# Performance work log

Hardware: AMD Instinct MI355X
Metric: run time of the kernel (lower is better)

The kernel has to match this reference:

```python
import jax, jax.numpy as jnp
import numpy as np

B, CIN, COUT, S, K, G = 2, 64, 64, 128, 3, 4  # batch, in_ch, out_ch, shapes(H=W), kernel, groups


def _conv1x1(w, x, b=None):
    # nn.Conv2d(kernel_size=1): w [O,C], x [B,C,H,W]
    y = jnp.einsum('oc,bchw->bohw', w, x)
    return y if b is None else y + b[None, :, None, None]


def _forward(fs, ft, w_q, w_k, w_v, rel_h, rel_w, weights1_real, weights1_imag,
             w0_w, w0_b, convv_w, convv_b, convv1_w, convv1_b, rate1, rate2):
    Bq, C, H, W = fs.shape
    q = _conv1x1(w_q, fs)  # [B,C,H,W]
    # key/value convs are 1x1 with no bias, so conv(pad(x)) == pad(conv(x))
    kf = jnp.pad(_conv1x1(w_k, fs), ((0, 0), (0, 0), (1, 1), (1, 1)))
    vf = jnp.pad(_conv1x1(w_v, fs), ((0, 0), (0, 0), (1, 1), (1, 1)))

    def unfold(xp):  # [B,C,H+2,W+2] -> [B,C,H,W,K,K] (torch .unfold(2,K,1).unfold(3,K,1))
        p = jnp.stack([xp[:, :, i:i + H, j:j + W] for i in range(K) for j in range(K)], axis=-1)
        return p.reshape(Bq, C, H, W, K, K)

    k = unfold(kf)
    v = unfold(vf)
    # relative position bias on the two channel halves (broadcast as in torch)
    k = jnp.concatenate([k[:, :C // 2] + rel_h, k[:, C // 2:] + rel_w], axis=1)
    k = k.reshape(Bq, G, C // G, H, W, K * K)
    v = v.reshape(Bq, G, C // G, H, W, K * K)
    qg = q.reshape(Bq, G, C // G, H, W, 1)
    attn = jax.nn.softmax(qg * k, axis=-1)                         # [B,G,C/G,H,W,9]
    out = jnp.einsum('bnchwk,bnchwk->bnchw', attn, v).reshape(Bq, C, H, W)

    # ---- spectral branch ----
    # Original code: einsum 'bchw,ohwi->bochw' (i is summed over weights only),
    # flatten to [B, o*c*H, W], fftshift over dims(1,2), reshape to [B,64,8192,128,2],
    # zero an EMPTY slice (rw=int(0.1*1)=0), ifftshift over dims(3,2,1), then
    # ifft2 with s=(H,W) which CROPS the 8192 dim to its first H rows.
    # The roll arithmetic composes to: net-zero shift on o and w axes, and a
    # +C/2 shift on the c axis; the crop then selects c = C//2, h = 0..H-1.
    # => out1 = Re ifft2( fft2(out)[:, C//2] * sum_i W[o,:,h,w] ).
    fs_ft = jnp.fft.fft2(out, norm='ortho')                        # [B,C,H,W] complex
    wsum = (weights1_real + 1j * weights1_imag).sum(axis=1)        # [CIN,H,W] (sum over 'i')
    out_ft = fs_ft[:, C // 2][:, None, :, :] * wsum[None]          # [B,CIN,H,W]
    out1 = jnp.fft.ifft2(out_ft, norm='ortho').real                # [B,CIN,H,W]

    out_cv = _conv1x1(convv_w, out, convv_b)                       # con_vv
    out2 = _conv1x1(w0_w, out_cv, w0_b)                            # w0
    out2 = _conv1x1(convv1_w, out2, convv1_b)                      # con_vv1

    make_fs = rate1[0] * out1 + rate2[0] * out2                    # [B,CIN,H,W]
    make_fs = jnp.transpose(make_fs, (0, 2, 3, 1))                 # [B,H,W,C]
    ftv = ft.reshape(Bq, H, W, C)                                  # out_channels != 320 branch
    return jnp.mean((make_fs - ftv) ** 2)


def setup_inputs() -> dict:
    key = jax.random.key(0)
    ks = jax.random.split(key, 12)
    n = lambda i, shape, s=1.0: jax.random.normal(ks[i], shape, dtype=jnp.float32) * s
    scale = 1.0 / (CIN * COUT)
    return {
        'fs': n(0, (B, CIN, S, S)),
        'ft': n(1, (B, S, S, COUT)),
        'w_q': n(2, (COUT, CIN), 0.1),
        'w_k': n(3, (COUT, CIN), 0.1),
        'w_v': n(4, (COUT, CIN), 0.1),
        'rel_h': n(5, (COUT // 2, 1, 1, K, 1)),
        'rel_w': n(6, (COUT // 2, 1, 1, 1, K)),
        'weights1_real': jax.random.uniform(ks[7], (CIN, COUT, S, S), dtype=jnp.float32) * scale,
        'weights1_imag': jax.random.uniform(ks[8], (CIN, COUT, S, S), dtype=jnp.float32) * scale,
        'w0_w': n(9, (COUT, CIN), 0.1),
        'w0_b': jnp.zeros((COUT,), jnp.float32),
        'convv_w': n(10, (CIN, COUT), 0.1),
        'convv_b': jnp.zeros((CIN,), jnp.float32),
        'convv1_w': n(11, (CIN, COUT), 0.1),
        'convv1_b': jnp.zeros((CIN,), jnp.float32),
        'rate1': jnp.full((1,), 0.5, jnp.float32),
        'rate2': jnp.full((1,), 0.5, jnp.float32),
    }


def reference(fs, ft, w_q, w_k, w_v, rel_h, rel_w, weights1_real, weights1_imag,
              w0_w, w0_b, convv_w, convv_b, convv1_w, convv1_b, rate1, rate2):
    return _forward(fs, ft, w_q, w_k, w_v, rel_h, rel_w, weights1_real, weights1_imag,
                    w0_w, w0_b, convv_w, convv_b, convv1_w, convv1_b, rate1, rate2)
```

## Files before the change

### kernel.cpp

```cpp
#include <hip/hip_runtime.h>
#include <math.h>

constexpr int HW   = 128 * 128;
constexpr int NCHW = 2 * 64 * HW;

constexpr size_t OFF_Q    = 0;
constexpr size_t OFF_K    = 2097152;
constexpr size_t OFF_V    = 4194304;
constexpr size_t OFF_OUT  = 6291456;
constexpr size_t OFF_OUT2 = 8388608;
constexpr size_t OFF_R    = 8388608;
constexpr size_t OFF_F    = 10485760;
constexpr size_t OFF_M    = 10551296;
constexpr size_t OFF_BC   = 10555392;
constexpr size_t OFF_Z    = 0;
constexpr size_t OFF_P    = 4194304;

__global__ __launch_bounds__(256) void k_qkv(
    const float* __restrict__ fs,
    const float* __restrict__ w_q, const float* __restrict__ w_k, const float* __restrict__ w_v,
    float* __restrict__ q, float* __restrict__ kk, float* __restrict__ vv)
{
    __shared__ float xs[64][64];
    __shared__ float wl[3][64][65];
    int blk = blockIdx.x;
    int b = blk >> 8;
    int px0 = (blk & 255) << 6;
    int t = threadIdx.x;
    for (int i = t; i < 4096; i += 256) {
        int r = i >> 6, cix = i & 63;
        wl[0][r][cix] = w_q[i];
        wl[1][r][cix] = w_k[i];
        wl[2][r][cix] = w_v[i];
        xs[r][cix] = fs[b * (64 * HW) + r * HW + px0 + cix];
    }
    __syncthreads();
    int pxq = t & 15, rq = t >> 4;
    float aq[4][4], ak[4][4], av[4][4];
    #pragma unroll
    for (int i = 0; i < 4; i++)
        for (int j = 0; j < 4; j++) { aq[i][j] = 0.f; ak[i][j] = 0.f; av[i][j] = 0.f; }
    for (int ci = 0; ci < 64; ci++) {
        float4 xv = *reinterpret_cast<const float4*>(&xs[ci][pxq * 4]);
        #pragma unroll
        for (int i = 0; i < 4; i++) {
            float wq_ = wl[0][rq * 4 + i][ci];
            float wk_ = wl[1][rq * 4 + i][ci];
            float wv_ = wl[2][rq * 4 + i][ci];
            aq[i][0] += wq_ * xv.x; aq[i][1] += wq_ * xv.y; aq[i][2] += wq_ * xv.z; aq[i][3] += wq_ * xv.w;
            ak[i][0] += wk_ * xv.x; ak[i][1] += wk_ * xv.y; ak[i][2] += wk_ * xv.z; ak[i][3] += wk_ * xv.w;
            av[i][0] += wv_ * xv.x; av[i][1] += wv_ * xv.y; av[i][2] += wv_ * xv.z; av[i][3] += wv_ * xv.w;
        }
    }
    #pragma unroll
    for (int i = 0; i < 4; i++) {
        int co = rq * 4 + i;
        size_t base = (size_t)b * (64 * HW) + (size_t)co * HW + px0 + pxq * 4;
        *reinterpret_cast<float4*>(q  + base) = make_float4(aq[i][0], aq[i][1], aq[i][2], aq[i][3]);
        *reinterpret_cast<float4*>(kk + base) = make_float4(ak[i][0], ak[i][1], ak[i][2], ak[i][3]);
        *reinterpret_cast<float4*>(vv + base) = make_float4(av[i][0], av[i][1], av[i][2], av[i][3]);
    }
}

__global__ __launch_bounds__(256) void k_gemm64(
    const float* __restrict__ x, const float* __restrict__ w,
    const float* __restrict__ bias, float* __restrict__ y)
{
    __shared__ float xs[64][64];
    __shared__ float wl[64][65];
    int blk = blockIdx.x;
    int b = blk >> 8;
    int px0 = (blk & 255) << 6;
    int t = threadIdx.x;
    for (int i = t; i < 4096; i += 256) {
        int r = i >> 6, cix = i & 63;
        wl[r][cix] = w[i];
        xs[r][cix] = x[b * (64 * HW) + r * HW + px0 + cix];
    }
    __syncthreads();
    int pxq = t & 15, rq = t >> 4;
    float acc[4][4];
    #pragma unroll
    for (int i = 0; i < 4; i++)
        for (int j = 0; j < 4; j++) acc[i][j] = 0.f;
    for (int ci = 0; ci < 64; ci++) {
        float4 xv = *reinterpret_cast<const float4*>(&xs[ci][pxq * 4]);
        #pragma unroll
        for (int i = 0; i < 4; i++) {
            float wv = wl[rq * 4 + i][ci];
            acc[i][0] += wv * xv.x; acc[i][1] += wv * xv.y;
            acc[i][2] += wv * xv.z; acc[i][3] += wv * xv.w;
        }
    }
    #pragma unroll
    for (int i = 0; i < 4; i++) {
        int co = rq * 4 + i;
        float bb = bias ? bias[co] : 0.f;
        float* p = y + b * (64 * HW) + co * HW + px0 + pxq * 4;
        p[0] = acc[i][0] + bb; p[1] = acc[i][1] + bb;
        p[2] = acc[i][2] + bb; p[3] = acc[i][3] + bb;
    }
}

__global__ __launch_bounds__(256) void k_attn(
    const float* __restrict__ q, const float* __restrict__ kc, const float* __restrict__ vc,
    const float* __restrict__ rel_h, const float* __restrict__ rel_w,
    float* __restrict__ out)
{
    int idx = blockIdx.x * 256 + threadIdx.x;
    if (idx >= NCHW) return;
    int w = idx & 127;
    int h = (idx >> 7) & 127;
    int c = (idx >> 14) & 63;
    float qv = q[idx];
    float s[9], vv[9];
    #pragma unroll
    for (int ki = 0; ki < 3; ki++) {
        #pragma unroll
        for (int kj = 0; kj < 3; kj++) {
            int hh = h + ki - 1, ww = w + kj - 1;
            bool inb = (hh >= 0 && hh < 128 && ww >= 0 && ww < 128);
            int nidx = (idx & ~(HW - 1)) + hh * 128 + ww;
            float kvv = inb ? kc[nidx] : 0.f;
            float vvv = inb ? vc[nidx] : 0.f;
            float rel = (c < 32) ? rel_h[c * 3 + ki] : rel_w[(c - 32) * 3 + kj];
            s[ki * 3 + kj] = qv * (kvv + rel);
            vv[ki * 3 + kj] = vvv;
        }
    }
    float m = s[0];
    #pragma unroll
    for (int i = 1; i < 9; i++) m = fmaxf(m, s[i]);
    float den = 0.f, num = 0.f;
    #pragma unroll
    for (int i = 0; i < 9; i++) { float e = __expf(s[i] - m); den += e; num += e * vv[i]; }
    out[idx] = num / den;
}

__global__ __launch_bounds__(128) void k_fftrow_fwd(const float* __restrict__ out, float* __restrict__ R)
{
    int bh = blockIdx.x; int b = bh >> 7, h = bh & 127;
    int k = threadIdx.x;
    __shared__ float xr[128];
    xr[k] = out[((b * 64 + 32) << 14) + h * 128 + k];
    __syncthreads();
    float s0, c0; __sincosf(-6.2831853071795864769f * (float)k / 128.0f, &s0, &c0);
    float twr = 1.f, twi = 0.f, ar = 0.f, ai = 0.f;
    for (int n = 0; n < 128; n++) {
        float xv = xr[n];
        ar += xv * twr; ai += xv * twi;
        float nr = twr * c0 - twi * s0;
        twi = twr * s0 + twi * c0; twr = nr;
    }
    float2* Rp = (float2*)R;
    Rp[(b << 14) + h * 128 + k] = make_float2(ar, ai);
}

__global__ __launch_bounds__(128) void k_fftcol_fwd(const float* __restrict__ R, float* __restrict__ F)
{
    int bk = blockIdx.x; int b = bk >> 7, k2 = bk & 127;
    int k1 = threadIdx.x;
    __shared__ float2 col[128];
    const float2* Rp = (const float2*)R;
    col[k1] = Rp[(b << 14) + k1 * 128 + k2];
    __syncthreads();
    float s0, c0; __sincosf(-6.2831853071795864769f * (float)k1 / 128.0f, &s0, &c0);
    float twr = 1.f, twi = 0.f, ar = 0.f, ai = 0.f;
    for (int n = 0; n < 128; n++) {
        float2 xv = col[n];
        ar += xv.x * twr - xv.y * twi;
        ai += xv.x * twi + xv.y * twr;
        float nr = twr * c0 - twi * s0;
        twi = twr * s0 + twi * c0; twr = nr;
    }
    float2* Fp = (float2*)F;
    Fp[(b << 14) + k1 * 128 + k2] = make_float2(ar * (1.f / 128.f), ai * (1.f / 128.f));
}

__global__ __launch_bounds__(1024) void k_combine(
    const float* __restrict__ convv_w, const float* __restrict__ convv_b,
    const float* __restrict__ w0_w, const float* __restrict__ w0_b,
    const float* __restrict__ convv1_w, const float* __restrict__ convv1_b,
    float* __restrict__ M, float* __restrict__ bc)
{
    __shared__ float A[64][64];
    __shared__ float Bm[64][64];
    __shared__ float Cm[64][64];
    __shared__ float T[64][65];
    __shared__ float t2[64];
    int t = threadIdx.x;
    for (int e = t; e < 4096; e += 1024) {
        int i = e >> 6, j = e & 63;
        A[i][j]  = convv_w[e];
        Bm[i][j] = w0_w[e];
        Cm[i][j] = convv1_w[e];
    }
    __syncthreads();
    for (int e = t; e < 4096; e += 1024) {
        int i = e >> 6, j = e & 63;
        float a = 0.f;
        for (int kk = 0; kk < 64; kk++) a += Bm[i][kk] * A[kk][j];
        T[i][j] = a;
    }
    if (t < 64) {
        float a = 0.f;
        for (int kk = 0; kk < 64; kk++) a += Bm[t][kk] * convv_b[kk];
        t2[t] = a + w0_b[t];
    }
    __syncthreads();
    for (int e = t; e < 4096; e += 1024) {
        int i = e >> 6, j = e & 63;
        float a = 0.f;
        for (int kk = 0; kk < 64; kk++) a += Cm[i][kk] * T[kk][j];
        M[e] = a;
    }
    if (t < 64) {
        float a = 0.f;
        for (int kk = 0; kk < 64; kk++) a += Cm[t][kk] * t2[kk];
        bc[t] = a + convv1_b[t];
    }
}

__global__ __launch_bounds__(256) void k_wsum_partial(
    const float* __restrict__ w1r, const float* __restrict__ w1i, float* __restrict__ P)
{
    int blk = blockIdx.x;
    int chunk = blk & 15;
    int half  = (blk >> 4) & 1;
    int c     = blk >> 5;
    int t = threadIdx.x;
    int hw4 = (chunk << 8) + t;
    size_t base4 = ((size_t)c << 18) + ((size_t)half << 17) + (size_t)hw4;
    const float4* r4 = reinterpret_cast<const float4*>(w1r) + base4;
    const float4* i4 = reinterpret_cast<const float4*>(w1i) + base4;
    float4 sr = make_float4(0.f, 0.f, 0.f, 0.f);
    float4 si = make_float4(0.f, 0.f, 0.f, 0.f);
    #pragma unroll 16
    for (int o = 0; o < 32; o++) {
        float4 a = r4[o << 12];
        float4 b = i4[o << 12];
        sr.x += a.x; sr.y += a.y; sr.z += a.z; sr.w += a.w;
        si.x += b.x; si.y += b.y; si.z += b.z; si.w += b.w;
    }
    float2* Pp = reinterpret_cast<float2*>(P);
    size_t ob = ((size_t)half << 20) + ((size_t)c << 14) + (size_t)hw4 * 4;
    Pp[ob + 0] = make_float2(sr.x, si.x);
    Pp[ob + 1] = make_float2(sr.y, si.y);
    Pp[ob + 2] = make_float2(sr.z, si.z);
    Pp[ob + 3] = make_float2(sr.w, si.w);
}

__global__ __launch_bounds__(128) void k_ifftrow(
    const float* __restrict__ P, const float* __restrict__ F, float* __restrict__ Z)
{
    int blk = blockIdx.x; int c = blk >> 7, h = blk & 127;
    int t = threadIdx.x;
    __shared__ float2 g0[128];
    __shared__ float2 g1[128];
    const float2* Pp = (const float2*)P;
    const float2* Fp = (const float2*)F;
    float2 p0 = Pp[((size_t)c << 14) + (h << 7) + t];
    float2 p1 = Pp[((size_t)1 << 20) + ((size_t)c << 14) + (h << 7) + t];
    float wr = p0.x + p1.x, wi = p0.y + p1.y;
    float2 f0 = Fp[(h << 7) + t];
    float2 f1 = Fp[(1 << 14) + (h << 7) + t];
    g0[t] = make_float2(f0.x * wr - f0.y * wi, f0.x * wi + f0.y * wr);
    g1[t] = make_float2(f1.x * wr - f1.y * wi, f1.x * wi + f1.y * wr);
    __syncthreads();
    float s0, c0; __sincosf(6.2831853071795864769f * (float)t / 128.0f, &s0, &c0);
    float twr = 1.f, twi = 0.f;
    float a0r = 0.f, a0i = 0.f, a1r = 0.f, a1i = 0.f;
    for (int n = 0; n < 128; n++) {
        float2 u0 = g0[n];
        float2 u1 = g1[n];
        a0r += u0.x * twr - u0.y * twi;
        a0i += u0.x * twi + u0.y * twr;
        a1r += u1.x * twr - u1.y * twi;
        a1i += u1.x * twi + u1.y * twr;
        float nr = twr * c0 - twi * s0;
        twi = twr * s0 + twi * c0; twr = nr;
    }
    float2* Zp = (float2*)Z;
    Zp[((size_t)c << 14) + h * 128 + t]        = make_float2(a0r, a0i);
    Zp[((size_t)(64 + c) << 14) + h * 128 + t] = make_float2(a1r, a1i);
}

__global__ __launch_bounds__(256) void k_ifftcol_mse(
    const float* __restrict__ Zb, const float* __restrict__ out2,
    const float* __restrict__ ft, const float* __restrict__ rate1,
    const float* __restrict__ rate2, float* __restrict__ result)
{
    int blk = blockIdx.x;
    int xc = blk & 3;
    int c  = (blk >> 2) & 63;
    int b  = blk >> 8;
    int t = threadIdx.x;
    int xl = t & 31;
    int yq = t >> 5;
    __shared__ float2 zs[128][33];
    const float2* Zp = (const float2*)Zb;
    int zbase = ((b * 64 + c) << 14) + xc * 32;
    for (int e = t; e < 4096; e += 256) {
        int hh = e >> 5, xx = e & 31;
        zs[hh][xx] = Zp[zbase + hh * 128 + xx];
    }
    __syncthreads();

    float twx[4], twy[4], stx[4], sty[4];
    float Sr[4][4], Si[4][4];
    #pragma unroll
    for (int j = 0; j < 4; j++) {
        int y0 = yq + 8 * j;
        float ss, cc;
        __sincosf(6.2831853071795864769f * (float)y0 / 128.0f, &ss, &cc);
        stx[j] = cc; sty[j] = ss;
        twx[j] = 1.f; twy[j] = 0.f;
        #pragma unroll
        for (int m = 0; m < 4; m++) { Sr[j][m] = 0.f; Si[j][m] = 0.f; }
    }
    for (int h = 0; h < 128; h += 4) {
        #pragma unroll
        for (int m = 0; m < 4; m++) {
            float2 z = zs[h + m][xl];
            #pragma unroll
            for (int j = 0; j < 4; j++) {
                Sr[j][m] += z.x * twx[j] - z.y * twy[j];
                Si[j][m] += z.x * twy[j] + z.y * twx[j];
                float nr = twx[j] * stx[j] - twy[j] * sty[j];
                twy[j]   = twx[j] * sty[j] + twy[j] * stx[j];
                twx[j]   = nr;
            }
        }
    }
    float r1 = rate1[0], r2 = rate2[0];
    int x = xc * 32 + xl;
    int obase = ((b * 64 + c) << 14) + x;
    float part = 0.f;
    #pragma unroll
    for (int j = 0; j < 4; j++) {
        int y0 = yq + 8 * j;
        float o[4];
        o[0] = Sr[j][0] + Sr[j][1] + Sr[j][2] + Sr[j][3];
        o[1] = Sr[j][0] - Si[j][1] - Sr[j][2] + Si[j][3];
        o[2] = Sr[j][0] - Sr[j][1] + Sr[j][2] - Sr[j][3];
        o[3] = Sr[j][0] + Si[j][1] - Sr[j][2] - Si[j][3];
        #pragma unroll
        for (int m = 0; m < 4; m++) {
            int y = y0 + 32 * m;
            float out1 = o[m] * (1.f / 128.f);
            int gi = obase + y * 128;
            float mk = r1 * out1 + r2 * out2[gi];
            int fidx = ((b * HW + y * 128 + x) << 6) + c;
            float d = mk - ft[fidx];
            part += d * d;
        }
    }
    __shared__ float red[256];
    red[t] = part;
    __syncthreads();
    for (int s = 128; s > 0; s >>= 1) {
        if (t < s) red[t] += red[t + s];
        __syncthreads();
    }
    if (t == 0) atomicAdd(result, red[0] * (1.f / 2097152.f));
}

extern "C" void kernel_launch(void* const* d_in, const int* in_sizes, int n_in,
                              void* d_out, int out_size, void* d_ws, size_t ws_size,
                              hipStream_t stream) {
    const float* fs       = (const float*)d_in[0];
    const float* ft       = (const float*)d_in[1];
    const float* w_q      = (const float*)d_in[2];
    const float* w_k      = (const float*)d_in[3];
    const float* w_v      = (const float*)d_in[4];
    const float* rel_h    = (const float*)d_in[5];
    const float* rel_w    = (const float*)d_in[6];
    const float* w1r      = (const float*)d_in[7];
    const float* w1i      = (const float*)d_in[8];
    const float* w0_w     = (const float*)d_in[9];
    const float* w0_b     = (const float*)d_in[10];
    const float* convv_w  = (const float*)d_in[11];
    const float* convv_b  = (const float*)d_in[12];
    const float* convv1_w = (const float*)d_in[13];
    const float* convv1_b = (const float*)d_in[14];
    const float* rate1    = (const float*)d_in[15];
    const float* rate2    = (const float*)d_in[16];

    float* ws = (float*)d_ws;
    float* q    = ws + OFF_Q;
    float* kk   = ws + OFF_K;
    float* vv   = ws + OFF_V;
    float* out  = ws + OFF_OUT;
    float* out2 = ws + OFF_OUT2;
    float* R    = ws + OFF_R;
    float* F    = ws + OFF_F;
    float* M    = ws + OFF_M;
    float* bc   = ws + OFF_BC;
    float* Z    = ws + OFF_Z;
    float* P    = ws + OFF_P;

    k_qkv<<<512, 256, 0, stream>>>(fs, w_q, w_k, w_v, q, kk, vv);
    k_attn<<<8192, 256, 0, stream>>>(q, kk, vv, rel_h, rel_w, out);
    k_fftrow_fwd<<<256, 128, 0, stream>>>(out, R);
    k_fftcol_fwd<<<256, 128, 0, stream>>>(R, F);
    k_combine<<<1, 1024, 0, stream>>>(convv_w, convv_b, w0_w, w0_b, convv1_w, convv1_b, M, bc);
    k_gemm64<<<512, 256, 0, stream>>>(out, M, bc, out2);
    k_wsum_partial<<<2048, 256, 0, stream>>>(w1r, w1i, P);
    k_ifftrow<<<8192, 128, 0, stream>>>(P, F, Z);
    hipMemsetAsync(d_out, 0, sizeof(float), stream);
    k_ifftcol_mse<<<512, 256, 0, stream>>>(Z, out2, ft, rate1, rate2, (float*)d_out);
}
```

Baseline: 705.0 us.

## Fuse weight-combine into row FFT launch and restructure wsum reduction loads

The single-block matrix-combine kernel is merged into the forward row-FFT kernel as an extra 257th block, removing one launch and letting the combine run concurrently with the FFT rows. Because that block now has 128 threads instead of 1024, its tail work is longer. The weight-sum reduction is reworked to issue eight independent float4 loads per iteration into four accumulator sets, with a per-block rotated starting phase to spread memory accesses. It also gets an occupancy hint in launch_bounds. This targets memory-level parallelism on the 64 MB weight read that likely dominates runtime.

```diff
diff --git a/kernel.cpp b/kernel.cpp
--- a/kernel.cpp
+++ b/kernel.cpp
@@ -137,23 +137,66 @@
     out[idx] = num / den;
 }
 
-__global__ __launch_bounds__(128) void k_fftrow_fwd(const float* __restrict__ out, float* __restrict__ R)
-{
-    int bh = blockIdx.x; int b = bh >> 7, h = bh & 127;
-    int k = threadIdx.x;
+__global__ __launch_bounds__(128) void k_fftrow_combine(
+    const float* __restrict__ out, float* __restrict__ R,
+    const float* __restrict__ convv_w, const float* __restrict__ convv_b,
+    const float* __restrict__ w0_w, const float* __restrict__ w0_b,
+    const float* __restrict__ convv1_w, const float* __restrict__ convv1_b,
+    float* __restrict__ M, float* __restrict__ bc)
+{
     __shared__ float xr[128];
-    xr[k] = out[((b * 64 + 32) << 14) + h * 128 + k];
-    __syncthreads();
-    float s0, c0; __sincosf(-6.2831853071795864769f * (float)k / 128.0f, &s0, &c0);
-    float twr = 1.f, twi = 0.f, ar = 0.f, ai = 0.f;
-    for (int n = 0; n < 128; n++) {
-        float xv = xr[n];
-        ar += xv * twr; ai += xv * twi;
-        float nr = twr * c0 - twi * s0;
-        twi = twr * s0 + twi * c0; twr = nr;
-    }
-    float2* Rp = (float2*)R;
-    Rp[(b << 14) + h * 128 + k] = make_float2(ar, ai);
+    __shared__ float A[64][64];
+    __shared__ float Bm[64][64];
+    __shared__ float Cm[64][64];
+    __shared__ float T[64][65];
+    __shared__ float t2[64];
+    int t = threadIdx.x;
+    if (blockIdx.x < 256) {
+        int bh = blockIdx.x; int b = bh >> 7, h = bh & 127;
+        xr[t] = out[((b * 64 + 32) << 14) + h * 128 + t];
+        __syncthreads();
+        float s0, c0; __sincosf(-6.2831853071795864769f * (float)t / 128.0f, &s0, &c0);
+        float twr = 1.f, twi = 0.f, ar = 0.f, ai = 0.f;
+        for (int n = 0; n < 128; n++) {
+            float xv = xr[n];
+            ar += xv * twr; ai += xv * twi;
+            float nr = twr * c0 - twi * s0;
+            twi = twr * s0 + twi * c0; twr = nr;
+        }
+        float2* Rp = (float2*)R;
+        Rp[(b << 14) + h * 128 + t] = make_float2(ar, ai);
+        return;
+    }
+    for (int e = t; e < 4096; e += 128) {
+        int i = e >> 6, j = e & 63;
+        A[i][j]  = convv_w[e];
+        Bm[i][j] = w0_w[e];
+        Cm[i][j] = convv1_w[e];
+    }
+    __syncthreads();
+    for (int e = t; e < 4096; e += 128) {
+        int i = e >> 6, j = e & 63;
+        float a = 0.f;
+        for (int kk = 0; kk < 64; kk++) a += Bm[i][kk] * A[kk][j];
+        T[i][j] = a;
+    }
+    if (t < 64) {
+        float a = 0.f;
+        for (int kk = 0; kk < 64; kk++) a += Bm[t][kk] * convv_b[kk];
+        t2[t] = a + w0_b[t];
+    }
+    __syncthreads();
+    for (int e = t; e < 4096; e += 128) {
+        int i = e >> 6, j = e & 63;
+        float a = 0.f;
+        for (int kk = 0; kk < 64; kk++) a += Cm[i][kk] * T[kk][j];
+        M[e] = a;
+    }
+    if (t < 64) {
+        float a = 0.f;
+        for (int kk = 0; kk < 64; kk++) a += Cm[t][kk] * t2[kk];
+        bc[t] = a + convv1_b[t];
+    }
 }
 
 __global__ __launch_bounds__(128) void k_fftcol_fwd(const float* __restrict__ R, float* __restrict__ F)
@@ -177,51 +220,7 @@
     Fp[(b << 14) + k1 * 128 + k2] = make_float2(ar * (1.f / 128.f), ai * (1.f / 128.f));
 }
 
-__global__ __launch_bounds__(1024) void k_combine(
-    const float* __restrict__ convv_w, const float* __restrict__ convv_b,
-    const float* __restrict__ w0_w, const float* __restrict__ w0_b,
-    const float* __restrict__ convv1_w, const float* __restrict__ convv1_b,
-    float* __restrict__ M, float* __restrict__ bc)
-{
-    __shared__ float A[64][64];
-    __shared__ float Bm[64][64];
-    __shared__ float Cm[64][64];
-    __shared__ float T[64][65];
-    __shared__ float t2[64];
-    int t = threadIdx.x;
-    for (int e = t; e < 4096; e += 1024) {
-        int i = e >> 6, j = e & 63;
-        A[i][j]  = convv_w[e];
-        Bm[i][j] = w0_w[e];
-        Cm[i][j] = convv1_w[e];
-    }
-    __syncthreads();
-    for (int e = t; e < 4096; e += 1024) {
-        int i = e >> 6, j = e & 63;
-        float a = 0.f;
-        for (int kk = 0; kk < 64; kk++) a += Bm[i][kk] * A[kk][j];
-        T[i][j] = a;
-    }
-    if (t < 64) {
-        float a = 0.f;
-        for (int kk = 0; kk < 64; kk++) a += Bm[t][kk] * convv_b[kk];
-        t2[t] = a + w0_b[t];
-    }
-    __syncthreads();
-    for (int e = t; e < 4096; e += 1024) {
-        int i = e >> 6, j = e & 63;
-        float a = 0.f;
-        for (int kk = 0; kk < 64; kk++) a += Cm[i][kk] * T[kk][j];
-        M[e] = a;
-    }
-    if (t < 64) {
-        float a = 0.f;
-        for (int kk = 0; kk < 64; kk++) a += Cm[t][kk] * t2[kk];
-        bc[t] = a + convv1_b[t];
-    }
-}
-
-__global__ __launch_bounds__(256) void k_wsum_partial(
+__global__ __launch_bounds__(256, 4) void k_wsum_partial(
     const float* __restrict__ w1r, const float* __restrict__ w1i, float* __restrict__ P)
 {
     int blk = blockIdx.x;
@@ -233,21 +232,44 @@
     size_t base4 = ((size_t)c << 18) + ((size_t)half << 17) + (size_t)hw4;
     const float4* r4 = reinterpret_cast<const float4*>(w1r) + base4;
     const float4* i4 = reinterpret_cast<const float4*>(w1i) + base4;
-    float4 sr = make_float4(0.f, 0.f, 0.f, 0.f);
-    float4 si = make_float4(0.f, 0.f, 0.f, 0.f);
-    #pragma unroll 16
-    for (int o = 0; o < 32; o++) {
-        float4 a = r4[o << 12];
-        float4 b = i4[o << 12];
-        sr.x += a.x; sr.y += a.y; sr.z += a.z; sr.w += a.w;
-        si.x += b.x; si.y += b.y; si.z += b.z; si.w += b.w;
-    }
+    int phase = (chunk + c * 3 + half * 5) & 7;
+    float4 aR0 = make_float4(0.f,0.f,0.f,0.f), aR1 = aR0, aR2 = aR0, aR3 = aR0;
+    float4 aI0 = aR0, aI1 = aR0, aI2 = aR0, aI3 = aR0;
+    #pragma unroll
+    for (int oo = 0; oo < 8; oo++) {
+        int g = (oo + phase) & 7;
+        size_t ob = (size_t)(g << 2) << 12;
+        float4 r0 = r4[ob];
+        float4 r1 = r4[ob + 4096];
+        float4 r2 = r4[ob + 8192];
+        float4 r3 = r4[ob + 12288];
+        float4 s0 = i4[ob];
+        float4 s1 = i4[ob + 4096];
+        float4 s2 = i4[ob + 8192];
+        float4 s3 = i4[ob + 12288];
+        aR0.x += r0.x; aR0.y += r0.y; aR0.z += r0.z; aR0.w += r0.w;
+        aR1.x += r1.x; aR1.y += r1.y; aR1.z += r1.z; aR1.w += r1.w;
+        aR2.x += r2.x; aR2.y += r2.y; aR2.z += r2.z; aR2.w += r2.w;
+        aR3.x += r3.x; aR3.y += r3.y; aR3.z += r3.z; aR3.w += r3.w;
+        aI0.x += s0.x; aI0.y += s0.y; aI0.z += s0.z; aI0.w += s0.w;
+        aI1.x += s1.x; aI1.y += s1.y; aI1.z += s1.z; aI1.w += s1.w;
+        aI2.x += s2.x; aI2.y += s2.y; aI2.z += s2.z; aI2.w += s2.w;
+        aI3.x += s3.x; aI3.y += s3.y; aI3.z += s3.z; aI3.w += s3.w;
+    }
+    float4 sr = make_float4(aR0.x + aR1.x + aR2.x + aR3.x,
+                            aR0.y + aR1.y + aR2.y + aR3.y,
+                            aR0.z + aR1.z + aR2.z + aR3.z,
+                            aR0.w + aR1.w + aR2.w + aR3.w);
+    float4 si = make_float4(aI0.x + aI1.x + aI2.x + aI3.x,
+                            aI0.y + aI1.y + aI2.y + aI3.y,
+                            aI0.z + aI1.z + aI2.z + aI3.z,
+                            aI0.w + aI1.w + aI2.w + aI3.w);
     float2* Pp = reinterpret_cast<float2*>(P);
-    size_t ob = ((size_t)half << 20) + ((size_t)c << 14) + (size_t)hw4 * 4;
-    Pp[ob + 0] = make_float2(sr.x, si.x);
-    Pp[ob + 1] = make_float2(sr.y, si.y);
-    Pp[ob + 2] = make_float2(sr.z, si.z);
-    Pp[ob + 3] = make_float2(sr.w, si.w);
+    size_t ob2 = ((size_t)half << 20) + ((size_t)c << 14) + (size_t)hw4 * 4;
+    Pp[ob2 + 0] = make_float2(sr.x, si.x);
+    Pp[ob2 + 1] = make_float2(sr.y, si.y);
+    Pp[ob2 + 2] = make_float2(sr.z, si.z);
+    Pp[ob2 + 3] = make_float2(sr.w, si.w);
 }
 
 __global__ __launch_bounds__(128) void k_ifftrow(
@@ -401,9 +423,9 @@
 
     k_qkv<<<512, 256, 0, stream>>>(fs, w_q, w_k, w_v, q, kk, vv);
     k_attn<<<8192, 256, 0, stream>>>(q, kk, vv, rel_h, rel_w, out);
-    k_fftrow_fwd<<<256, 128, 0, stream>>>(out, R);
+    k_fftrow_combine<<<257, 128, 0, stream>>>(out, R, convv_w, convv_b, w0_w, w0_b,
+                                              convv1_w, convv1_b, M, bc);
     k_fftcol_fwd<<<256, 128, 0, stream>>>(R, F);
-    k_combine<<<1, 1024, 0, stream>>>(convv_w, convv_b, w0_w, w0_b, convv1_w, convv1_b, M, bc);
     k_gemm64<<<512, 256, 0, stream>>>(out, M, bc, out2);
     k_wsum_partial<<<2048, 256, 0, stream>>>(w1r, w1i, P);
     k_ifftrow<<<8192, 128, 0, stream>>>(P, F, Z);
```

Measured after the change: 852.2 us. 1.21x slower.

## Restructure spectral weight reduction into LDS-accumulated quarter sums and alias Z buffer

Applied to the files above, without the earlier changes.

The reduction of weights1 over the output-channel axis is restructured. It now uses 256 blocks of 512 threads, and each block accumulates 16 channels into 128KB of shared-memory accumulators. This produces four partial sums per input channel instead of two. The row inverse-FFT kernel adds the four partials and writes its results in place over the partial buffer, so the separate Z workspace is no longer needed. The main cost is a large streaming read. Holding one big block per CU cuts occupancy and memory-level parallelism, which may hurt throughput on that bandwidth-bound read.

```diff
diff --git a/kernel.cpp b/kernel.cpp
--- a/kernel.cpp
+++ b/kernel.cpp
@@ -13,8 +13,7 @@
 constexpr size_t OFF_F    = 10485760;
 constexpr size_t OFF_M    = 10551296;
 constexpr size_t OFF_BC   = 10555392;
-constexpr size_t OFF_Z    = 0;
-constexpr size_t OFF_P    = 4194304;
+constexpr size_t OFF_P    = 0;
 
 __global__ __launch_bounds__(256) void k_qkv(
     const float* __restrict__ fs,
@@ -221,47 +220,60 @@
     }
 }
 
-__global__ __launch_bounds__(256) void k_wsum_partial(
+__global__ __launch_bounds__(512) void k_wsum(
     const float* __restrict__ w1r, const float* __restrict__ w1i, float* __restrict__ P)
 {
+    __shared__ float accR[4][4096];
+    __shared__ float accI[4][4096];
     int blk = blockIdx.x;
-    int chunk = blk & 15;
-    int half  = (blk >> 4) & 1;
-    int c     = blk >> 5;
-    int t = threadIdx.x;
-    int hw4 = (chunk << 8) + t;
-    size_t base4 = ((size_t)c << 18) + ((size_t)half << 17) + (size_t)hw4;
-    const float4* r4 = reinterpret_cast<const float4*>(w1r) + base4;
-    const float4* i4 = reinterpret_cast<const float4*>(w1i) + base4;
-    float4 sr = make_float4(0.f, 0.f, 0.f, 0.f);
-    float4 si = make_float4(0.f, 0.f, 0.f, 0.f);
-    #pragma unroll 16
-    for (int o = 0; o < 32; o++) {
-        float4 a = r4[o << 12];
-        float4 b = i4[o << 12];
-        sr.x += a.x; sr.y += a.y; sr.z += a.z; sr.w += a.w;
-        si.x += b.x; si.y += b.y; si.z += b.z; si.w += b.w;
+    int oq = blk & 3, c = blk >> 2;
+    int t = threadIdx.x;
+    #pragma unroll
+    for (int k = 0; k < 8; ++k) {
+        int s = t + (k << 9);
+        accR[0][s] = 0.f; accR[1][s] = 0.f; accR[2][s] = 0.f; accR[3][s] = 0.f;
+        accI[0][s] = 0.f; accI[1][s] = 0.f; accI[2][s] = 0.f; accI[3][s] = 0.f;
+    }
+    const float4* r4 = reinterpret_cast<const float4*>(w1r) + ((size_t)(c * 64 + oq * 16) << 12);
+    const float4* i4 = reinterpret_cast<const float4*>(w1i) + ((size_t)(c * 64 + oq * 16) << 12);
+    for (int o = 0; o < 16; ++o) {
+        #pragma unroll
+        for (int k = 0; k < 8; ++k) {
+            int s = t + (k << 9);
+            float4 a = r4[(o << 12) + s];
+            float4 b = i4[(o << 12) + s];
+            accR[0][s] += a.x; accR[1][s] += a.y; accR[2][s] += a.z; accR[3][s] += a.w;
+            accI[0][s] += b.x; accI[1][s] += b.y; accI[2][s] += b.z; accI[3][s] += b.w;
+        }
     }
     float2* Pp = reinterpret_cast<float2*>(P);
-    size_t ob = ((size_t)half << 20) + ((size_t)c << 14) + (size_t)hw4 * 4;
-    Pp[ob + 0] = make_float2(sr.x, si.x);
-    Pp[ob + 1] = make_float2(sr.y, si.y);
-    Pp[ob + 2] = make_float2(sr.z, si.z);
-    Pp[ob + 3] = make_float2(sr.w, si.w);
+    size_t base = (size_t)((c << 2) + oq) << 14;
+    #pragma unroll
+    for (int k = 0; k < 8; ++k) {
+        int s = t + (k << 9);
+        Pp[base + (s << 2) + 0] = make_float2(accR[0][s], accI[0][s]);
+        Pp[base + (s << 2) + 1] = make_float2(accR[1][s], accI[1][s]);
+        Pp[base + (s << 2) + 2] = make_float2(accR[2][s], accI[2][s]);
+        Pp[base + (s << 2) + 3] = make_float2(accR[3][s], accI[3][s]);
+    }
 }
 
 __global__ __launch_bounds__(128) void k_ifftrow(
-    const float* __restrict__ P, const float* __restrict__ F, float* __restrict__ Z)
+    float* __restrict__ P, const float* __restrict__ F)
 {
     int blk = blockIdx.x; int c = blk >> 7, h = blk & 127;
     int t = threadIdx.x;
     __shared__ float2 g0[128];
     __shared__ float2 g1[128];
-    const float2* Pp = (const float2*)P;
+    float2* Pp = (float2*)P;
     const float2* Fp = (const float2*)F;
-    float2 p0 = Pp[((size_t)c << 14) + (h << 7) + t];
-    float2 p1 = Pp[((size_t)1 << 20) + ((size_t)c << 14) + (h << 7) + t];
-    float wr = p0.x + p1.x, wi = p0.y + p1.y;
+    size_t rowoff = (size_t)(h << 7) + t;
+    float2 p0 = Pp[((size_t)((c << 2) + 0) << 14) + rowoff];
+    float2 p1 = Pp[((size_t)((c << 2) + 1) << 14) + rowoff];
+    float2 p2 = Pp[((size_t)((c << 2) + 2) << 14) + rowoff];
+    float2 p3 = Pp[((size_t)((c << 2) + 3) << 14) + rowoff];
+    float wr = p0.x + p1.x + p2.x + p3.x;
+    float wi = p0.y + p1.y + p2.y + p3.y;
     float2 f0 = Fp[(h << 7) + t];
     float2 f1 = Fp[(1 << 14) + (h << 7) + t];
     g0[t] = make_float2(f0.x * wr - f0.y * wi, f0.x * wi + f0.y * wr);
@@ -280,9 +292,8 @@
         float nr = twr * c0 - twi * s0;
         twi = twr * s0 + twi * c0; twr = nr;
     }
-    float2* Zp = (float2*)Z;
-    Zp[((size_t)c << 14) + h * 128 + t]        = make_float2(a0r, a0i);
-    Zp[((size_t)(64 + c) << 14) + h * 128 + t] = make_float2(a1r, a1i);
+    Pp[((size_t)((c << 2) + 0) << 14) + rowoff] = make_float2(a0r, a0i);
+    Pp[((size_t)((c << 2) + 1) << 14) + rowoff] = make_float2(a1r, a1i);
 }
 
 __global__ __launch_bounds__(256) void k_ifftcol_mse(
@@ -299,7 +310,7 @@
     int yq = t >> 5;
     __shared__ float2 zs[128][33];
     const float2* Zp = (const float2*)Zb;
-    int zbase = ((b * 64 + c) << 14) + xc * 32;
+    size_t zbase = ((size_t)((c << 2) + b) << 14) + xc * 32;
     for (int e = t; e < 4096; e += 256) {
         int hh = e >> 5, xx = e & 31;
         zs[hh][xx] = Zp[zbase + hh * 128 + xx];
@@ -396,7 +407,6 @@
     float* F    = ws + OFF_F;
     float* M    = ws + OFF_M;
     float* bc   = ws + OFF_BC;
-    float* Z    = ws + OFF_Z;
     float* P    = ws + OFF_P;
 
     k_qkv<<<512, 256, 0, stream>>>(fs, w_q, w_k, w_v, q, kk, vv);
@@ -405,8 +415,8 @@
     k_fftcol_fwd<<<256, 128, 0, stream>>>(R, F);
     k_combine<<<1, 1024, 0, stream>>>(convv_w, convv_b, w0_w, w0_b, convv1_w, convv1_b, M, bc);
     k_gemm64<<<512, 256, 0, stream>>>(out, M, bc, out2);
-    k_wsum_partial<<<2048, 256, 0, stream>>>(w1r, w1i, P);
-    k_ifftrow<<<8192, 128, 0, stream>>>(P, F, Z);
+    k_wsum<<<256, 512, 0, stream>>>(w1r, w1i, P);
+    k_ifftrow<<<8192, 128, 0, stream>>>(P, F);
     hipMemsetAsync(d_out, 0, sizeof(float), stream);
-    k_ifftcol_mse<<<512, 256, 0, stream>>>(Z, out2, ft, rate1, rate2, (float*)d_out);
-}
+    k_ifftcol_mse<<<512, 256, 0, stream>>>(P, out2, ft, rate1, rate2, (float*)d_out);
+}
```

Result: no change. 713.1 us (+1.1%).
